# Kernel tuning notes

Measured on AMD Instinct MI355X. Metric: run time of the kernel, lower is better.

## Reference

```python
import jax, jax.numpy as jnp
import numpy as np

K = 64                      # sort-pool k
B_GRAPHS, N_PER = 256, 512  # graphs, nodes per graph
DIM_F, E_PER = 128, 8192    # node feature dim, edges per graph
EMB = 32


def setup_inputs() -> dict:
    key = jax.random.key(0)
    ks = jax.random.split(key, 12)
    N = B_GRAPHS * N_PER
    off = (jnp.arange(B_GRAPHS) * N_PER)[:, None]
    x = jax.random.normal(ks[0], (N, DIM_F), jnp.float32)
    edge_src = (jax.random.randint(ks[1], (B_GRAPHS, E_PER), 0, N_PER) + off).reshape(-1)
    edge_dst = (jax.random.randint(ks[2], (B_GRAPHS, E_PER), 0, N_PER) + off).reshape(-1)

    def lin(k, o, i):
        return (jax.random.normal(k, (o, i), jnp.float32) / np.float32(np.sqrt(i)))

    return {
        "x": x,
        "W0": lin(ks[3], EMB, DIM_F), "b0": jnp.zeros((EMB,), jnp.float32),
        "W1": lin(ks[4], EMB, EMB),   "b1": jnp.zeros((EMB,), jnp.float32),
        "W2": lin(ks[5], EMB, EMB),   "b2": jnp.zeros((EMB,), jnp.float32),
        "W3": lin(ks[6], 1, EMB),     "b3": jnp.zeros((1,), jnp.float32),
        "conv1_w": jax.random.normal(ks[7], (16, 1, 97), jnp.float32) / np.float32(np.sqrt(97.0)),
        "conv1_b": jnp.zeros((16,), jnp.float32),
        "conv2_w": jax.random.normal(ks[8], (32, 16, 5), jnp.float32) / np.float32(np.sqrt(80.0)),
        "conv2_b": jnp.zeros((32,), jnp.float32),
        "d1_w": lin(ks[9], 128, 896),  "d1_b": jnp.zeros((128,), jnp.float32),
        "d2_w": lin(ks[10], 10, 128),  "d2_b": jnp.zeros((10,), jnp.float32),
        "edge_src": edge_src, "edge_dst": edge_dst,
        "num_graphs": B_GRAPHS,
    }


def _dgcnn_conv(h_in, W, b, src, dst):
    # h = lin(x); message = (1/deg_src)[dst] * h[src]; scatter-add at dst
    N = h_in.shape[0]
    h = h_in @ W.T + b
    deg = jax.ops.segment_sum(jnp.ones_like(src, dtype=h.dtype), src, num_segments=N)
    norm = 1.0 / deg                       # self-loops guarantee deg >= 1
    msg = h[src] * norm[dst][:, None]      # [E+N, C]
    return jax.ops.segment_sum(msg, dst, num_segments=N)


def _forward(x, W0, b0, W1, b1, W2, b2, W3, b3,
             conv1_w, conv1_b, conv2_w, conv2_b,
             d1_w, d1_b, d2_w, d2_b, src, dst, num_graphs):
    N = x.shape[0]
    self_idx = jnp.arange(N)
    src = jnp.concatenate([src, self_idx])   # add_self_loops
    dst = jnp.concatenate([dst, self_idx])
    hs = []
    h = x
    for (W, b) in ((W0, b0), (W1, b1), (W2, b2), (W3, b3)):
        h = jnp.tanh(_dgcnn_conv(h, W, b, src, dst))
        hs.append(h)
    feat = jnp.concatenate(hs, axis=1)       # [N, 97]
    D = feat.shape[1]
    B = num_graphs
    n = N // B
    g = feat.reshape(B, n, D)
    # global_sort_pool: sort nodes per graph by last channel, descending, take top-k
    order = jnp.argsort(-g[:, :, -1], axis=1)[:, :K]
    topk = jnp.take_along_axis(g, order[:, :, None], axis=1)   # [B, K, D]
    # Conv1d(1,16,kernel=D,stride=D) over [B,1,K*D] == per-node linear on D
    c1 = jax.nn.relu(jnp.einsum('bkd,od->bok', topk, conv1_w[:, 0, :])
                     + conv1_b[None, :, None])                  # [B,16,K]
    p = c1.reshape(B, 16, K // 2, 2).max(axis=-1)               # MaxPool1d(2,2)
    c2 = jax.lax.conv_general_dilated(p, conv2_w, (1,), 'VALID',
                                      dimension_numbers=('NCH', 'OIH', 'NCH'))
    c2 = jax.nn.relu(c2 + conv2_b[None, :, None])               # [B,32,28]
    flat = c2.reshape(B, -1)                                    # [B,896]
    hid = jax.nn.relu(flat @ d1_w.T + d1_b)                     # dropout = identity (eval)
    return hid @ d2_w.T + d2_b                                  # [B,10]


def reference(x, W0, b0, W1, b1, W2, b2, W3, b3,
              conv1_w, conv1_b, conv2_w, conv2_b,
              d1_w, d1_b, d2_w, d2_b, edge_src, edge_dst, num_graphs):
    return _forward(x, W0, b0, W1, b1, W2, b2, W3, b3,
                    conv1_w, conv1_b, conv2_w, conv2_b,
                    d1_w, d1_b, d2_w, d2_b, edge_src, edge_dst, num_graphs)
```

## Files before the change

### kernel.cpp

```cpp
#include <hip/hip_runtime.h>

#define NG   256
#define NP   512
#define EPG  8192
#define FDIM 128
#define STB  34

#define OFF_BUFB 0
#define OFF_CSR  69632
#define OFF_OFFS (OFF_CSR + 16384)
#define OFF_WT   (OFF_OFFS + 1028)
#define OFF_CUR  (OFF_WT + 32)
#define OFF_DCNT (OFF_CUR + 2048)
#define OFF_NRM  (OFF_DCNT + 2048)
#define OFF_L3   (OFF_NRM + 2048)
#define SMEM_SZ  (OFF_L3 + 2048)

#define OFF_KEY  OFF_CSR
#define OFF_IDX  (OFF_CSR + 2048)
#define FO_C1   (97*64)
#define FO_P    (FO_C1 + 16*64)
#define FO_C2   (FO_P + 16*32)
#define FO_HID  (FO_C2 + 896)

__global__ __launch_bounds__(1024, 4) void dgcnn_fused(
    const float* __restrict__ x,
    const float* __restrict__ W0, const float* __restrict__ b0,
    const float* __restrict__ W1, const float* __restrict__ b1,
    const float* __restrict__ W2, const float* __restrict__ b2,
    const float* __restrict__ W3, const float* __restrict__ b3,
    const float* __restrict__ c1w, const float* __restrict__ c1b,
    const float* __restrict__ c2w, const float* __restrict__ c2b,
    const float* __restrict__ d1w, const float* __restrict__ d1b,
    const float* __restrict__ d2w, const float* __restrict__ d2b,
    const int* __restrict__ esrc, const int* __restrict__ edst,
    float* __restrict__ hs1, float* __restrict__ hs2,
    float* __restrict__ out)
{
  extern __shared__ char smem[];
  float*          bufB  = (float*)(smem + OFF_BUFB);
  unsigned short* csr   = (unsigned short*)(smem + OFF_CSR);
  unsigned short* offs  = (unsigned short*)(smem + OFF_OFFS);
  unsigned int*   wt    = (unsigned int*)(smem + OFF_WT);
  unsigned int*   cur   = (unsigned int*)(smem + OFF_CUR);
  unsigned int*   dcnt  = (unsigned int*)(smem + OFF_DCNT);
  float*          nrm   = (float*)(smem + OFF_NRM);
  float*          lin3S = (float*)(smem + OFF_L3);
  float*          keyA  = (float*)(smem + OFF_KEY);
  unsigned int*   idxA  = (unsigned int*)(smem + OFF_IDX);
  float*          featS = bufB;

  const int g    = blockIdx.x;
  const int tid  = threadIdx.x;
  const int lane = tid & 63;
  const int wv   = __builtin_amdgcn_readfirstlane(tid >> 6);
  const int half = __builtin_amdgcn_readfirstlane(tid >> 9);
  const int v    = tid & 511;
  const int nb   = g * NP;
  const size_t gb = (size_t)g * (NP * 32);

  if (tid < 512) { cur[tid] = 0u; dcnt[tid] = 0u; }
  __syncthreads();

  int es[8], ed[8];
  {
    const int eb = g * EPG;
#pragma unroll
    for (int i = 0; i < 8; i++) {
      const int e = eb + tid + i * 1024;
      es[i] = esrc[e] - nb;
      ed[i] = edst[e] - nb;
    }
#pragma unroll
    for (int i = 0; i < 8; i++) {
      atomicAdd(&dcnt[es[i]], 1u);
      atomicAdd(&dcnt[ed[i]], 65536u);
    }
  }
  __syncthreads();

  unsigned c_scan = 0;
  if (tid < 512) {
    const unsigned cw = dcnt[tid];
    nrm[tid] = 1.0f / (float)((cw & 0xFFFFu) + 1u);
    c_scan = cw >> 16;
    for (int d = 1; d < 64; d <<= 1) {
      const unsigned t = __shfl_up(c_scan, (unsigned)d, 64);
      if (lane >= d) c_scan += t;
    }
    if (lane == 63) wt[wv] = c_scan;
  }
  __syncthreads();
  if (tid < 512) {
    unsigned base = 0;
    for (int w = 0; w < wv; w++) base += wt[w];
    offs[tid + 1] = (unsigned short)(base + c_scan);
    if (tid == 0) offs[0] = 0;
  }
  __syncthreads();

#pragma unroll
  for (int i = 0; i < 8; i++) {
    const unsigned pos = (unsigned)offs[ed[i]] + atomicAdd(&cur[ed[i]], 1u);
    csr[pos] = (unsigned short)es[i];
  }
  __syncthreads();

  {
    const float* xr = x + (size_t)(nb + v) * FDIM;
    float acc[16];
#pragma unroll
    for (int c = 0; c < 16; c++) acc[c] = b0[half * 16 + c];
    for (int kb = 0; kb < 4; kb++) {
      float4 xv[8];
      const float4* xq = (const float4*)(xr + kb * 32);
#pragma unroll
      for (int j = 0; j < 8; j++) xv[j] = xq[j];
#pragma unroll
      for (int c = 0; c < 16; c++) {
        const float* wr = W0 + (size_t)(half * 16 + c) * FDIM + kb * 32;
        float a = acc[c];
#pragma unroll
        for (int j = 0; j < 8; j++) {
          a = fmaf(xv[j].x, wr[j*4+0], a);
          a = fmaf(xv[j].y, wr[j*4+1], a);
          a = fmaf(xv[j].z, wr[j*4+2], a);
          a = fmaf(xv[j].w, wr[j*4+3], a);
        }
        acc[c] = a;
      }
    }
    float4* br = (float4*)(bufB + v * STB + half * 16);
#pragma unroll
    for (int j = 0; j < 4; j++)
      br[j] = make_float4(acc[j*4+0], acc[j*4+1], acc[j*4+2], acc[j*4+3]);
  }
  __syncthreads();

  float h[16];
  auto do_agg = [&]() {
    float4 A0, A1, A2, A3;
    const float4* sr = (const float4*)(bufB + v * STB + half * 16);
    A0 = sr[0]; A1 = sr[1]; A2 = sr[2]; A3 = sr[3];
    const int e0 = offs[v], e1 = offs[v + 1];
    for (int e = e0; e < e1; e++) {
      const int s = csr[e];
      const float4* rb = (const float4*)(bufB + s * STB + half * 16);
      const float4 r0 = rb[0], r1 = rb[1], r2 = rb[2], r3 = rb[3];
      A0.x += r0.x; A0.y += r0.y; A0.z += r0.z; A0.w += r0.w;
      A1.x += r1.x; A1.y += r1.y; A1.z += r1.z; A1.w += r1.w;
      A2.x += r2.x; A2.y += r2.y; A2.z += r2.z; A2.w += r2.w;
      A3.x += r3.x; A3.y += r3.y; A3.z += r3.z; A3.w += r3.w;
    }
    const float nv = nrm[v];
    h[0]=tanhf(A0.x*nv); h[1]=tanhf(A0.y*nv); h[2]=tanhf(A0.z*nv); h[3]=tanhf(A0.w*nv);
    h[4]=tanhf(A1.x*nv); h[5]=tanhf(A1.y*nv); h[6]=tanhf(A1.z*nv); h[7]=tanhf(A1.w*nv);
    h[8]=tanhf(A2.x*nv); h[9]=tanhf(A2.y*nv); h[10]=tanhf(A2.z*nv); h[11]=tanhf(A2.w*nv);
    h[12]=tanhf(A3.x*nv); h[13]=tanhf(A3.y*nv); h[14]=tanhf(A3.z*nv); h[15]=tanhf(A3.w*nv);
  };

  auto put_h = [&]() {
    float4* br = (float4*)(bufB + v * STB + half * 16);
#pragma unroll
    for (int j = 0; j < 4; j++)
      br[j] = make_float4(h[j*4+0], h[j*4+1], h[j*4+2], h[j*4+3]);
  };

  auto spill = [&](float* dst) {
#pragma unroll
    for (int c = 0; c < 16; c++)
      dst[gb + (size_t)(half * 16 + c) * 512 + v] = h[c];
  };

  auto do_lin = [&](const float* __restrict__ W, const float* __restrict__ b) {
    float hf[32];
    const float4* rr = (const float4*)(bufB + v * STB);
#pragma unroll
    for (int j = 0; j < 8; j++) {
      const float4 t = rr[j];
      hf[j*4+0]=t.x; hf[j*4+1]=t.y; hf[j*4+2]=t.z; hf[j*4+3]=t.w;
    }
    __syncthreads();
    float acc[16];
#pragma unroll
    for (int c = 0; c < 16; c++) {
      const int C = half * 16 + c;
      const float* wr = W + C * 32;
      float a = b[C];
#pragma unroll
      for (int j = 0; j < 32; j++) a = fmaf(hf[j], wr[j], a);
      acc[c] = a;
    }
    float4* br = (float4*)(bufB + v * STB + half * 16);
#pragma unroll
    for (int j = 0; j < 4; j++)
      br[j] = make_float4(acc[j*4+0], acc[j*4+1], acc[j*4+2], acc[j*4+3]);
    __syncthreads();
  };

  do_agg();
  __syncthreads();
  put_h(); spill(hs1);
  __syncthreads();
  do_lin(W1, b1);
  do_agg();
  __syncthreads();
  put_h(); spill(hs2);
  __syncthreads();
  do_lin(W2, b2);
  do_agg();
  __syncthreads();
  put_h();
  __syncthreads();

  if (tid < 512) {
    const float4* rr = (const float4*)(bufB + tid * STB);
    double a = (double)b3[0];
#pragma unroll
    for (int j = 0; j < 8; j++) {
      const float4 t = rr[j];
      a = fma((double)t.x, (double)W3[j*4+0], a);
      a = fma((double)t.y, (double)W3[j*4+1], a);
      a = fma((double)t.z, (double)W3[j*4+2], a);
      a = fma((double)t.w, (double)W3[j*4+3], a);
    }
    lin3S[tid] = (float)a;
  }
  __syncthreads();
  float h4 = 0.f;
  if (tid < 512) {
    double a = (double)lin3S[tid];
    const int e0 = offs[tid], e1 = offs[tid + 1];
    for (int e = e0; e < e1; e++) a += (double)lin3S[csr[e]];
    a *= (double)nrm[tid];
    h4 = tanhf((float)a);
  }
  __syncthreads();
  if (tid < 512) { keyA[tid] = h4; idxA[tid] = (unsigned)tid; }

  for (int k = 2; k <= NP; k <<= 1) {
    for (int j = k >> 1; j > 0; j >>= 1) {
      __syncthreads();
      if (tid < 512) {
        const int i = tid;
        const int l = i ^ j;
        if (l > i) {
          const float    ki = keyA[i], kl = keyA[l];
          const unsigned ii = idxA[i], il = idxA[l];
          const bool iBeforeL = (ki > kl) || (ki == kl && ii < il);
          const bool doSwap = ((i & k) == 0) ? (!iBeforeL) : iBeforeL;
          if (doSwap) {
            keyA[i] = kl; keyA[l] = ki;
            idxA[i] = il; idxA[l] = ii;
          }
        }
      }
    }
  }
  __syncthreads();

  {
    const int k = tid >> 4, t = tid & 15;
    const int node = (int)idxA[k];
    float vals[7];
#pragma unroll
    for (int m = 0; m < 7; m++) {
      const int d = t + 16 * m;
      float val = 0.f;
      if (d < 32)       val = hs1[gb + (size_t)d * 512 + node];
      else if (d < 64)  val = hs2[gb + (size_t)(d - 32) * 512 + node];
      else if (d < 96)  val = bufB[node * STB + (d - 64)];
      else if (d == 96) val = keyA[k];
      vals[m] = val;
    }
    __syncthreads();
#pragma unroll
    for (int m = 0; m < 7; m++) {
      const int d = t + 16 * m;
      if (d < 97) featS[d * 64 + k] = vals[m];
    }
  }
  __syncthreads();

  {
    float* c1s = bufB + FO_C1;
    const int ch = wv;
    double a = (double)c1b[ch];
    const float* wr = c1w + ch * 97;
    for (int d = 0; d < 97; d++)
      a = fma((double)featS[d * 64 + lane], (double)wr[d], a);
    c1s[ch * 64 + lane] = fmaxf((float)a, 0.f);
  }
  __syncthreads();

  if (tid < 512) {
    float* c1s = bufB + FO_C1;
    float* ps  = bufB + FO_P;
    const int o = tid >> 5, jj = tid & 31;
    ps[o * 32 + jj] = fmaxf(c1s[o * 64 + 2 * jj], c1s[o * 64 + 2 * jj + 1]);
  }
  __syncthreads();

  {
    float* ps  = bufB + FO_P;
    float* c2s = bufB + FO_C2;
    const int o = wv;
    if (lane < 28) {
      double a0 = 0., a1 = 0.;
      for (int i = 0; i < 16; i++) {
#pragma unroll
        for (int r = 0; r < 5; r++) {
          const double pv = (double)ps[i * 32 + lane + r];
          a0 = fma(pv, (double)c2w[((o     ) * 16 + i) * 5 + r], a0);
          a1 = fma(pv, (double)c2w[((o + 16) * 16 + i) * 5 + r], a1);
        }
      }
      c2s[(o     ) * 28 + lane] = fmaxf((float)(a0 + (double)c2b[o     ]), 0.f);
      c2s[(o + 16) * 28 + lane] = fmaxf((float)(a1 + (double)c2b[o + 16]), 0.f);
    }
  }
  __syncthreads();

  {
    float* c2s  = bufB + FO_C2;
    float* hids = bufB + FO_HID;
    float fl[14];
#pragma unroll
    for (int j = 0; j < 14; j++) fl[j] = c2s[lane + j * 64];
    for (int hh = 0; hh < 8; hh++) {
      const int hI = wv * 8 + hh;
      const float* wr = d1w + (size_t)hI * 896;
      double a = 0.;
#pragma unroll
      for (int j = 0; j < 14; j++) a = fma((double)fl[j], (double)wr[lane + j * 64], a);
#pragma unroll
      for (int m = 32; m > 0; m >>= 1) a += __shfl_xor(a, m, 64);
      if (lane == 0) hids[hI] = fmaxf((float)(a + (double)d1b[hI]), 0.f);
    }
  }
  __syncthreads();

  if (tid < 10) {
    const float* hids = bufB + FO_HID;
    const float* wr = d2w + tid * 128;
    double a = (double)d2b[tid];
#pragma unroll 8
    for (int hh = 0; hh < 128; hh++) a = fma((double)hids[hh], (double)wr[hh], a);
    out[g * 10 + tid] = (float)a;
  }
}

extern "C" void kernel_launch(void* const* d_in, const int* in_sizes, int n_in,
                              void* d_out, int out_size, void* d_ws, size_t ws_size,
                              hipStream_t stream) {
  const float* x   = (const float*)d_in[0];
  const float* W0  = (const float*)d_in[1];
  const float* b0  = (const float*)d_in[2];
  const float* W1  = (const float*)d_in[3];
  const float* b1  = (const float*)d_in[4];
  const float* W2  = (const float*)d_in[5];
  const float* b2  = (const float*)d_in[6];
  const float* W3  = (const float*)d_in[7];
  const float* b3  = (const float*)d_in[8];
  const float* c1w = (const float*)d_in[9];
  const float* c1b = (const float*)d_in[10];
  const float* c2w = (const float*)d_in[11];
  const float* c2b = (const float*)d_in[12];
  const float* d1w = (const float*)d_in[13];
  const float* d1b = (const float*)d_in[14];
  const float* d2w = (const float*)d_in[15];
  const float* d2b = (const float*)d_in[16];
  const int* esrc  = (const int*)d_in[17];
  const int* edst  = (const int*)d_in[18];

  float* hs1 = (float*)d_ws;
  float* hs2 = hs1 + (size_t)NG * NP * 32;
  float* outp = (float*)d_out;

  hipFuncSetAttribute(reinterpret_cast<const void*>(dgcnn_fused),
                      hipFuncAttributeMaxDynamicSharedMemorySize, SMEM_SZ);
  dgcnn_fused<<<NG, 1024, SMEM_SZ, stream>>>(x, W0, b0, W1, b1, W2, b2, W3, b3,
                                             c1w, c1b, c2w, c2b, d1w, d1b, d2w, d2b,
                                             esrc, edst, hs1, hs2, outp);
}
```

Before: 335.7 us.

## Stage x tiles through swizzled LDS with prefetch, vectorize edge loads, unroll aggregation

The first linear layer now loads x through a coalesced, XOR-swizzled LDS staging buffer in 32-column chunks. The next chunk is prefetched into registers while the current one is consumed, replacing strided per-thread row reads from global memory. Edge index loads become int4 vector loads, and the neighbour aggregation loop is unrolled by two. The LDS layout is reorganised: row stride goes to 36, and the sort-pool feature and tail buffers move into the staging region so one sync can be dropped. The cost is a larger shared-memory footprint (about 163 KB), which limits each CU to one block and adds barriers inside the chunk loop.

```diff
diff --git a/kernel.cpp b/kernel.cpp
--- a/kernel.cpp
+++ b/kernel.cpp
@@ -4,24 +4,26 @@
 #define NP   512
 #define EPG  8192
 #define FDIM 128
-#define STB  34
-
-#define OFF_BUFB 0
-#define OFF_CSR  69632
-#define OFF_OFFS (OFF_CSR + 16384)
-#define OFF_WT   (OFF_OFFS + 1028)
-#define OFF_CUR  (OFF_WT + 32)
-#define OFF_DCNT (OFF_CUR + 2048)
-#define OFF_NRM  (OFF_DCNT + 2048)
-#define OFF_L3   (OFF_NRM + 2048)
-#define SMEM_SZ  (OFF_L3 + 2048)
+#define STB  36
+
+#define OFF_STAGE 0
+#define OFF_BUFB  65536
+#define OFF_CSR   139264
+#define OFF_OFFS  155648
+#define OFF_WT    156680
+#define OFF_CUR   156712
+#define OFF_DCNT  158760
+#define OFF_NRM   160808
+#define SMEM_SZ   162856
 
 #define OFF_KEY  OFF_CSR
 #define OFF_IDX  (OFF_CSR + 2048)
-#define FO_C1   (97*64)
-#define FO_P    (FO_C1 + 16*64)
-#define FO_C2   (FO_P + 16*32)
-#define FO_HID  (FO_C2 + 896)
+#define OFF_L3   OFF_CUR
+#define FO_FEAT 0
+#define FO_C1   6208
+#define FO_P    7232
+#define FO_C2   7744
+#define FO_HID  8640
 
 __global__ __launch_bounds__(1024, 4) void dgcnn_fused(
     const float* __restrict__ x,
@@ -38,6 +40,7 @@
     float* __restrict__ out)
 {
   extern __shared__ char smem[];
+  float*          stageF = (float*)(smem + OFF_STAGE);
   float*          bufB  = (float*)(smem + OFF_BUFB);
   unsigned short* csr   = (unsigned short*)(smem + OFF_CSR);
   unsigned short* offs  = (unsigned short*)(smem + OFF_OFFS);
@@ -48,7 +51,6 @@
   float*          lin3S = (float*)(smem + OFF_L3);
   float*          keyA  = (float*)(smem + OFF_KEY);
   unsigned int*   idxA  = (unsigned int*)(smem + OFF_IDX);
-  float*          featS = bufB;
 
   const int g    = blockIdx.x;
   const int tid  = threadIdx.x;
@@ -59,18 +61,38 @@
   const int nb   = g * NP;
   const size_t gb = (size_t)g * (NP * 32);
 
+  const int ldRow0 = tid >> 3;
+  const int ldGrp  = tid & 7;
+  const int ldSwz  = (ldGrp ^ (ldRow0 & 7)) * 16;
+  auto load_chunk = [&](int kc, float4* xr) {
+    const float* base = x + (size_t)nb * FDIM + kc * 32 + ldGrp * 4;
+#pragma unroll
+    for (int it = 0; it < 4; it++)
+      xr[it] = *(const float4*)(base + (size_t)(ldRow0 + it * 128) * FDIM);
+  };
+  auto store_chunk = [&](const float4* xr) {
+#pragma unroll
+    for (int it = 0; it < 4; it++)
+      *(float4*)(smem + OFF_STAGE + (ldRow0 + it * 128) * 128 + ldSwz) = xr[it];
+  };
+
+  float4 xr[4], xr2[4];
+  load_chunk(0, xr);
+
   if (tid < 512) { cur[tid] = 0u; dcnt[tid] = 0u; }
   __syncthreads();
 
   int es[8], ed[8];
   {
     const int eb = g * EPG;
-#pragma unroll
-    for (int i = 0; i < 8; i++) {
-      const int e = eb + tid + i * 1024;
-      es[i] = esrc[e] - nb;
-      ed[i] = edst[e] - nb;
-    }
+    const int4* s4 = (const int4*)(esrc + eb);
+    const int4* d4 = (const int4*)(edst + eb);
+    const int4 sa = s4[tid], sb = s4[tid + 1024];
+    const int4 da = d4[tid], db = d4[tid + 1024];
+    es[0]=sa.x-nb; es[1]=sa.y-nb; es[2]=sa.z-nb; es[3]=sa.w-nb;
+    es[4]=sb.x-nb; es[5]=sb.y-nb; es[6]=sb.z-nb; es[7]=sb.w-nb;
+    ed[0]=da.x-nb; ed[1]=da.y-nb; ed[2]=da.z-nb; ed[3]=da.w-nb;
+    ed[4]=db.x-nb; ed[5]=db.y-nb; ed[6]=db.z-nb; ed[7]=db.w-nb;
 #pragma unroll
     for (int i = 0; i < 8; i++) {
       atomicAdd(&dcnt[es[i]], 1u);
@@ -104,36 +126,37 @@
     const unsigned pos = (unsigned)offs[ed[i]] + atomicAdd(&cur[ed[i]], 1u);
     csr[pos] = (unsigned short)es[i];
   }
-  __syncthreads();
-
-  {
-    const float* xr = x + (size_t)(nb + v) * FDIM;
-    float acc[16];
-#pragma unroll
-    for (int c = 0; c < 16; c++) acc[c] = b0[half * 16 + c];
-    for (int kb = 0; kb < 4; kb++) {
-      float4 xv[8];
-      const float4* xq = (const float4*)(xr + kb * 32);
-#pragma unroll
-      for (int j = 0; j < 8; j++) xv[j] = xq[j];
+
+  float acc0[16];
+#pragma unroll
+  for (int c = 0; c < 16; c++) acc0[c] = b0[half * 16 + c];
+  const char* rowp = smem + OFF_STAGE + v * 128;
+  const int vswz = v & 7;
+  for (int kc = 0; kc < 4; kc++) {
+    __syncthreads();
+    store_chunk(xr);
+    if (kc < 3) load_chunk(kc + 1, xr2);
+    __syncthreads();
+#pragma unroll
+    for (int jg = 0; jg < 8; jg++) {
+      const float4 t = *(const float4*)(rowp + ((jg ^ vswz) * 16));
 #pragma unroll
       for (int c = 0; c < 16; c++) {
-        const float* wr = W0 + (size_t)(half * 16 + c) * FDIM + kb * 32;
-        float a = acc[c];
-#pragma unroll
-        for (int j = 0; j < 8; j++) {
-          a = fmaf(xv[j].x, wr[j*4+0], a);
-          a = fmaf(xv[j].y, wr[j*4+1], a);
-          a = fmaf(xv[j].z, wr[j*4+2], a);
-          a = fmaf(xv[j].w, wr[j*4+3], a);
-        }
-        acc[c] = a;
+        const float* wr = W0 + (size_t)(half * 16 + c) * FDIM + kc * 32 + jg * 4;
+        acc0[c] = fmaf(t.x, wr[0], acc0[c]);
+        acc0[c] = fmaf(t.y, wr[1], acc0[c]);
+        acc0[c] = fmaf(t.z, wr[2], acc0[c]);
+        acc0[c] = fmaf(t.w, wr[3], acc0[c]);
       }
     }
+#pragma unroll
+    for (int it = 0; it < 4; it++) xr[it] = xr2[it];
+  }
+  {
     float4* br = (float4*)(bufB + v * STB + half * 16);
 #pragma unroll
     for (int j = 0; j < 4; j++)
-      br[j] = make_float4(acc[j*4+0], acc[j*4+1], acc[j*4+2], acc[j*4+3]);
+      br[j] = make_float4(acc0[j*4+0], acc0[j*4+1], acc0[j*4+2], acc0[j*4+3]);
   }
   __syncthreads();
 
@@ -143,7 +166,19 @@
     const float4* sr = (const float4*)(bufB + v * STB + half * 16);
     A0 = sr[0]; A1 = sr[1]; A2 = sr[2]; A3 = sr[3];
     const int e0 = offs[v], e1 = offs[v + 1];
-    for (int e = e0; e < e1; e++) {
+    int e = e0;
+    for (; e + 1 < e1; e += 2) {
+      const int s0 = csr[e], s1 = csr[e + 1];
+      const float4* rb0 = (const float4*)(bufB + s0 * STB + half * 16);
+      const float4* rb1 = (const float4*)(bufB + s1 * STB + half * 16);
+      const float4 p0 = rb0[0], p1 = rb0[1], p2 = rb0[2], p3 = rb0[3];
+      const float4 q0 = rb1[0], q1 = rb1[1], q2 = rb1[2], q3 = rb1[3];
+      A0.x += p0.x + q0.x; A0.y += p0.y + q0.y; A0.z += p0.z + q0.z; A0.w += p0.w + q0.w;
+      A1.x += p1.x + q1.x; A1.y += p1.y + q1.y; A1.z += p1.z + q1.z; A1.w += p1.w + q1.w;
+      A2.x += p2.x + q2.x; A2.y += p2.y + q2.y; A2.z += p2.z + q2.z; A2.w += p2.w + q2.w;
+      A3.x += p3.x + q3.x; A3.y += p3.y + q3.y; A3.z += p3.z + q3.z; A3.w += p3.w + q3.w;
+    }
+    if (e < e1) {
       const int s = csr[e];
       const float4* rb = (const float4*)(bufB + s * STB + half * 16);
       const float4 r0 = rb[0], r1 = rb[1], r2 = rb[2], r3 = rb[3];
@@ -260,30 +295,25 @@
   __syncthreads();
 
   {
+    float* featS = stageF + FO_FEAT;
     const int k = tid >> 4, t = tid & 15;
     const int node = (int)idxA[k];
-    float vals[7];
 #pragma unroll
     for (int m = 0; m < 7; m++) {
       const int d = t + 16 * m;
-      float val = 0.f;
+      float val;
       if (d < 32)       val = hs1[gb + (size_t)d * 512 + node];
       else if (d < 64)  val = hs2[gb + (size_t)(d - 32) * 512 + node];
       else if (d < 96)  val = bufB[node * STB + (d - 64)];
-      else if (d == 96) val = keyA[k];
-      vals[m] = val;
-    }
-    __syncthreads();
-#pragma unroll
-    for (int m = 0; m < 7; m++) {
-      const int d = t + 16 * m;
-      if (d < 97) featS[d * 64 + k] = vals[m];
-    }
-  }
-  __syncthreads();
-
-  {
-    float* c1s = bufB + FO_C1;
+      else              val = keyA[k];
+      if (d < 97) featS[d * 64 + k] = val;
+    }
+  }
+  __syncthreads();
+
+  {
+    const float* featS = stageF + FO_FEAT;
+    float* c1s = stageF + FO_C1;
     const int ch = wv;
     double a = (double)c1b[ch];
     const float* wr = c1w + ch * 97;
@@ -294,16 +324,16 @@
   __syncthreads();
 
   if (tid < 512) {
-    float* c1s = bufB + FO_C1;
-    float* ps  = bufB + FO_P;
+    const float* c1s = stageF + FO_C1;
+    float* ps  = stageF + FO_P;
     const int o = tid >> 5, jj = tid & 31;
     ps[o * 32 + jj] = fmaxf(c1s[o * 64 + 2 * jj], c1s[o * 64 + 2 * jj + 1]);
   }
   __syncthreads();
 
   {
-    float* ps  = bufB + FO_P;
-    float* c2s = bufB + FO_C2;
+    const float* ps  = stageF + FO_P;
+    float* c2s = stageF + FO_C2;
     const int o = wv;
     if (lane < 28) {
       double a0 = 0., a1 = 0.;
@@ -322,8 +352,8 @@
   __syncthreads();
 
   {
-    float* c2s  = bufB + FO_C2;
-    float* hids = bufB + FO_HID;
+    const float* c2s  = stageF + FO_C2;
+    float* hids = stageF + FO_HID;
     float fl[14];
 #pragma unroll
     for (int j = 0; j < 14; j++) fl[j] = c2s[lane + j * 64];
@@ -341,7 +371,7 @@
   __syncthreads();
 
   if (tid < 10) {
-    const float* hids = bufB + FO_HID;
+    const float* hids = stageF + FO_HID;
     const float* wr = d2w + tid * 128;
     double a = (double)d2b[tid];
 #pragma unroll 8
```

Measured after the change: 279.5 us. -16.8%, faster.
